# Kernel tuning notes

Measured on AMD Instinct MI355X. Metric: run time of the kernel, lower is better.

## Reference

```python
import jax, jax.numpy as jnp
import numpy as np

SCALE = 0.1  # FullAttention(0.1) binds scale positionally

def setup_inputs() -> dict:
    key = jax.random.key(0)
    k1, k2, k3, k4, k5 = jax.random.split(key, 5)
    B, H, L, E = 128, 16, 64, 128
    C = H * E  # in_channel = 2048
    return {
        "queries": jax.random.normal(k1, (B, H, L, E), dtype=jnp.float32),
        "keys": jax.random.normal(k2, (B, H, L, E), dtype=jnp.float32),
        "values": jax.random.normal(k3, (B, H, L, E), dtype=jnp.float32),
        "W": jax.random.normal(k4, (C, C), dtype=jnp.float32) * (1.0 / np.sqrt(C)),
        "b": jax.random.normal(k5, (C,), dtype=jnp.float32) * 0.01,
    }

def reference(queries, keys, values, W, b):
    # inputs are [B, H, L, E]; module permutes to [B, L, H, E]
    q = jnp.transpose(queries, (0, 2, 1, 3))  # blhe
    k = jnp.transpose(keys, (0, 2, 1, 3))     # bshe
    v = jnp.transpose(values, (0, 2, 1, 3))   # bshd
    scores = jnp.einsum('blhe,bshe->bhls', q, k)
    A = jax.nn.softmax(SCALE * scores, axis=-1)  # dropout is identity in eval
    V = jnp.einsum('bhls,bshd->blhd', A, v)
    B_, L, H, D = V.shape
    out = V.reshape(-1, 64, H * D)  # view(-1, 64, in_channel)
    return out @ W.T + b
```

## Files before the change

### kernel.cpp

```cpp
#include <hip/hip_runtime.h>
#include <hip/hip_bf16.h>
#include <stdint.h>

typedef __bf16 bf16_t;
typedef __bf16 bf16x4 __attribute__((ext_vector_type(4)));
typedef __bf16 bf16x8 __attribute__((ext_vector_type(8)));
typedef float  f32x4  __attribute__((ext_vector_type(4)));

#define AS1 __attribute__((address_space(1)))
#define AS3 __attribute__((address_space(3)))

__device__ __forceinline__ void gld_lds16(const void* gp, void* lp) {
    __builtin_amdgcn_global_load_lds((const AS1 unsigned int*)gp,
                                     (AS3 unsigned int*)lp, 16, 0, 0);
}

__device__ __forceinline__ bf16_t bhi(float v) { return (bf16_t)v; }
__device__ __forceinline__ bf16_t blo(float v) {
    return (bf16_t)(v - (float)((bf16_t)v));
}

__global__ __launch_bounds__(256) void wconv_kernel(const float* __restrict__ W,
                                                    bf16_t* __restrict__ Wb) {
    const int i = (blockIdx.x * 256 + threadIdx.x) * 4;
    const float4 f = *(const float4*)&W[i];
    bf16x4 v = { (bf16_t)f.x, (bf16_t)f.y, (bf16_t)f.z, (bf16_t)f.w };
    *(bf16x4*)&Wb[i] = v;
}

#define QK_LD 136
#define VT_LD 72
#define SF_LD 65

__global__ __launch_bounds__(256) void attn_kernel(const float* __restrict__ Q,
                                                   const float* __restrict__ K,
                                                   const float* __restrict__ V,
                                                   bf16_t* __restrict__ X) {
    __shared__ __align__(16) char smem[53248];
    bf16_t* Qs = (bf16_t*)smem;
    bf16_t* Ks = (bf16_t*)(smem + 17408);
    bf16_t* Vt = (bf16_t*)(smem + 34816);
    float*  Sf = (float*)smem;
    bf16_t* Ps = (bf16_t*)(smem + 17408);

    const int bh   = blockIdx.x;
    const int b    = bh >> 4;
    const int h    = bh & 15;
    const int t    = threadIdx.x;
    const int w    = t >> 6;
    const int lane = t & 63;
    const int row16 = lane & 15;
    const int quad  = lane >> 4;

    const float* Qg = Q + (size_t)bh * 8192;
    const float* Kg = K + (size_t)bh * 8192;
    const float* Vg = V + (size_t)bh * 8192;

    const int r  = t >> 2;
    const int c0 = (t & 3) * 32;

    float qv[32], kv[32];
#pragma unroll
    for (int j = 0; j < 8; ++j) {
        const int c = c0 + 4 * j;
        *(float4*)&qv[4 * j] = *(const float4*)&Qg[r * 128 + c];
        *(float4*)&kv[4 * j] = *(const float4*)&Kg[r * 128 + c];
        const float4 v4 = *(const float4*)&Vg[r * 128 + c];
        Vt[(c + 0) * VT_LD + r] = (bf16_t)v4.x;
        Vt[(c + 1) * VT_LD + r] = (bf16_t)v4.y;
        Vt[(c + 2) * VT_LD + r] = (bf16_t)v4.z;
        Vt[(c + 3) * VT_LD + r] = (bf16_t)v4.w;
    }

#define STAGE(slot, vals, CONV)                                            \
    {                                                                      \
        _Pragma("unroll")                                                  \
        for (int j = 0; j < 8; ++j) {                                      \
            const int c = c0 + 4 * j;                                      \
            bf16x4 o = { CONV(vals[4*j+0]), CONV(vals[4*j+1]),             \
                         CONV(vals[4*j+2]), CONV(vals[4*j+3]) };           \
            *(bf16x4*)&slot[r * QK_LD + c] = o;                            \
        }                                                                  \
    }

    f32x4 accS[4];
#pragma unroll
    for (int ni = 0; ni < 4; ++ni) accS[ni] = (f32x4){0.f, 0.f, 0.f, 0.f};

#define SCORE_PASS()                                                       \
    {                                                                      \
        _Pragma("unroll")                                                  \
        for (int kb = 0; kb < 4; ++kb) {                                   \
            const bf16x8 a = *(const bf16x8*)&Qs[(16*w + row16)*QK_LD + 32*kb + 8*quad]; \
            _Pragma("unroll")                                              \
            for (int ni = 0; ni < 4; ++ni) {                               \
                const bf16x8 bb = *(const bf16x8*)&Ks[(16*ni + row16)*QK_LD + 32*kb + 8*quad]; \
                accS[ni] = __builtin_amdgcn_mfma_f32_16x16x32_bf16(a, bb, accS[ni], 0, 0, 0); \
            }                                                              \
        }                                                                  \
    }

    STAGE(Qs, qv, bhi)
    STAGE(Ks, kv, bhi)
    __syncthreads();
    SCORE_PASS()
    __syncthreads();
    STAGE(Ks, kv, blo)
    __syncthreads();
    SCORE_PASS()
    __syncthreads();
    STAGE(Qs, qv, blo)
    __syncthreads();
    SCORE_PASS()
    __syncthreads();
    STAGE(Ks, kv, bhi)
    __syncthreads();
    SCORE_PASS()
    __syncthreads();

#pragma unroll
    for (int ni = 0; ni < 4; ++ni)
#pragma unroll
        for (int rr = 0; rr < 4; ++rr)
            Sf[(16 * w + 4 * quad + rr) * SF_LD + 16 * ni + row16] = accS[ni][rr];
    __syncthreads();

    {
        const int c16 = (t & 3) * 16;
        float x[16];
        float mx = -1e30f;
#pragma unroll
        for (int j = 0; j < 16; ++j) {
            x[j] = Sf[r * SF_LD + c16 + j] * 0.1f;
            mx = fmaxf(mx, x[j]);
        }
        mx = fmaxf(mx, __shfl_xor(mx, 1));
        mx = fmaxf(mx, __shfl_xor(mx, 2));
        float sum = 0.f;
#pragma unroll
        for (int j = 0; j < 16; ++j) {
            x[j] = exp2f((x[j] - mx) * 1.44269504088896f);
            sum += x[j];
        }
        sum += __shfl_xor(sum, 1);
        sum += __shfl_xor(sum, 2);
        const float inv = 1.0f / sum;
#pragma unroll
        for (int j4 = 0; j4 < 4; ++j4) {
            bf16x4 p = { (bf16_t)(x[4 * j4 + 0] * inv), (bf16_t)(x[4 * j4 + 1] * inv),
                         (bf16_t)(x[4 * j4 + 2] * inv), (bf16_t)(x[4 * j4 + 3] * inv) };
            *(bf16x4*)&Ps[r * VT_LD + c16 + 4 * j4] = p;
        }
    }
    __syncthreads();

    f32x4 accO[8];
#pragma unroll
    for (int ni = 0; ni < 8; ++ni) accO[ni] = (f32x4){0.f, 0.f, 0.f, 0.f};
#pragma unroll
    for (int kb = 0; kb < 2; ++kb) {
        const bf16x8 a = *(const bf16x8*)&Ps[(16 * w + row16) * VT_LD + 32 * kb + 8 * quad];
#pragma unroll
        for (int ni = 0; ni < 8; ++ni) {
            const bf16x8 bb = *(const bf16x8*)&Vt[(16 * ni + row16) * VT_LD + 32 * kb + 8 * quad];
            accO[ni] = __builtin_amdgcn_mfma_f32_16x16x32_bf16(a, bb, accO[ni], 0, 0, 0);
        }
    }

    bf16_t* Xrow = X + (size_t)b * 64 * 2048 + h * 128;
#pragma unroll
    for (int ni = 0; ni < 8; ++ni)
#pragma unroll
        for (int rr = 0; rr < 4; ++rr) {
            const int l = 16 * w + 4 * quad + rr;
            const int d = 16 * ni + row16;
            Xrow[(size_t)l * 2048 + d] = (bf16_t)accO[ni][rr];
        }
}

__global__ __launch_bounds__(256) void gemm_kernel(const bf16_t* __restrict__ X,
                                                   const bf16_t* __restrict__ Wb,
                                                   const float* __restrict__ bias,
                                                   float* __restrict__ out) {
    __shared__ bf16_t As[128 * 32];
    __shared__ bf16_t Bs[128 * 32];

    const int t    = threadIdx.x;
    const int w    = t >> 6;
    const int lane = t & 63;
    const int row16 = lane & 15;
    const int quad  = lane >> 4;
    const int m0 = blockIdx.y * 128;
    const int n0 = blockIdx.x * 128;
    const int wm = w >> 1;
    const int wn = w & 1;

    const int srow = 32 * w + (lane >> 2);
    const int scol = (lane & 3) * 8;
    const bf16_t* gA = X  + (size_t)(m0 + srow) * 2048 + scol;
    const bf16_t* gB = Wb + (size_t)(n0 + srow) * 2048 + scol;
    bf16_t* lA0 = &As[(32 * w) * 32];
    bf16_t* lA1 = &As[(32 * w + 16) * 32];
    bf16_t* lB0 = &Bs[(32 * w) * 32];
    bf16_t* lB1 = &Bs[(32 * w + 16) * 32];

    f32x4 acc[4][4];
#pragma unroll
    for (int mi = 0; mi < 4; ++mi)
#pragma unroll
        for (int ni = 0; ni < 4; ++ni) acc[mi][ni] = (f32x4){0.f, 0.f, 0.f, 0.f};

    for (int kb = 0; kb < 64; ++kb) {
        const int k0 = kb * 32;
        __syncthreads();
        gld_lds16(gA + k0, lA0);
        gld_lds16(gA + 16 * 2048 + k0, lA1);
        gld_lds16(gB + k0, lB0);
        gld_lds16(gB + 16 * 2048 + k0, lB1);
        __syncthreads();

        bf16x8 a[4], bb[4];
#pragma unroll
        for (int mi = 0; mi < 4; ++mi)
            a[mi] = *(const bf16x8*)&As[(64 * wm + 16 * mi + row16) * 32 + 8 * quad];
#pragma unroll
        for (int ni = 0; ni < 4; ++ni)
            bb[ni] = *(const bf16x8*)&Bs[(64 * wn + 16 * ni + row16) * 32 + 8 * quad];
#pragma unroll
        for (int mi = 0; mi < 4; ++mi)
#pragma unroll
            for (int ni = 0; ni < 4; ++ni)
                acc[mi][ni] = __builtin_amdgcn_mfma_f32_16x16x32_bf16(a[mi], bb[ni], acc[mi][ni], 0, 0, 0);
    }

    const int nb = n0 + 64 * wn;
    float br[4];
#pragma unroll
    for (int ni = 0; ni < 4; ++ni) br[ni] = bias[nb + 16 * ni + row16];
#pragma unroll
    for (int mi = 0; mi < 4; ++mi)
#pragma unroll
        for (int ni = 0; ni < 4; ++ni)
#pragma unroll
            for (int rr = 0; rr < 4; ++rr) {
                const int m = m0 + 64 * wm + 16 * mi + 4 * quad + rr;
                const int n = nb + 16 * ni + row16;
                out[(size_t)m * 2048 + n] = acc[mi][ni][rr] + br[ni];
            }
}

extern "C" void kernel_launch(void* const* d_in, const int* in_sizes, int n_in,
                              void* d_out, int out_size, void* d_ws, size_t ws_size,
                              hipStream_t stream) {
    const float* Q    = (const float*)d_in[0];
    const float* K    = (const float*)d_in[1];
    const float* V    = (const float*)d_in[2];
    const float* W    = (const float*)d_in[3];
    const float* bias = (const float*)d_in[4];

    bf16_t* Xws = (bf16_t*)d_ws;
    bf16_t* Wb  = (bf16_t*)((char*)d_ws + (size_t)8192 * 2048 * 2);
    float*  out = (float*)d_out;

    wconv_kernel<<<4096, 256, 0, stream>>>(W, Wb);
    attn_kernel<<<2048, 256, 0, stream>>>(Q, K, V, Xws);
    gemm_kernel<<<dim3(16, 64), 256, 0, stream>>>(Xws, Wb, bias, out);
}
```

Baseline: 325.0 us.

## Trim split-bf16 score passes, coalesce attention output, widen GEMM K-tile with swizzle

The attention kernel drops the lo×lo score pass, going from four MFMA passes to three (hi·hi, hi·lo, lo·hi). It also stages the output tile through LDS so global writes become 16-byte vector stores instead of scattered 2-byte stores. The GEMM doubles its K-tile to 64 with an XOR-swizzled LDS layout to avoid bank conflicts, halving the number of barrier pairs. It also swaps the grid order so consecutive blocks share a W column tile, and adds an occupancy hint. Dropping the lo×lo term slightly changes the score precision, which stays negligible at bf16-split accuracy.

```diff
diff --git a/kernel.cpp b/kernel.cpp
--- a/kernel.cpp
+++ b/kernel.cpp
@@ -42,6 +42,7 @@
     bf16_t* Vt = (bf16_t*)(smem + 34816);
     float*  Sf = (float*)smem;
     bf16_t* Ps = (bf16_t*)(smem + 17408);
+    bf16_t* Ob = (bf16_t*)smem;
 
     const int bh   = blockIdx.x;
     const int b    = bh >> 4;
@@ -101,19 +102,15 @@
     }
 
     STAGE(Qs, qv, bhi)
+    STAGE(Ks, kv, blo)
+    __syncthreads();
+    SCORE_PASS()
+    __syncthreads();
     STAGE(Ks, kv, bhi)
     __syncthreads();
     SCORE_PASS()
     __syncthreads();
-    STAGE(Ks, kv, blo)
-    __syncthreads();
-    SCORE_PASS()
-    __syncthreads();
     STAGE(Qs, qv, blo)
-    __syncthreads();
-    SCORE_PASS()
-    __syncthreads();
-    STAGE(Ks, kv, bhi)
     __syncthreads();
     SCORE_PASS()
     __syncthreads();
@@ -167,42 +164,57 @@
         }
     }
 
-    bf16_t* Xrow = X + (size_t)b * 64 * 2048 + h * 128;
 #pragma unroll
     for (int ni = 0; ni < 8; ++ni)
 #pragma unroll
-        for (int rr = 0; rr < 4; ++rr) {
-            const int l = 16 * w + 4 * quad + rr;
-            const int d = 16 * ni + row16;
-            Xrow[(size_t)l * 2048 + d] = (bf16_t)accO[ni][rr];
-        }
-}
-
-__global__ __launch_bounds__(256) void gemm_kernel(const bf16_t* __restrict__ X,
-                                                   const bf16_t* __restrict__ Wb,
-                                                   const float* __restrict__ bias,
-                                                   float* __restrict__ out) {
-    __shared__ bf16_t As[128 * 32];
-    __shared__ bf16_t Bs[128 * 32];
+        for (int rr = 0; rr < 4; ++rr)
+            Ob[(16 * w + 4 * quad + rr) * QK_LD + 16 * ni + row16] = (bf16_t)accO[ni][rr];
+    __syncthreads();
+
+    {
+        bf16_t* Xrow = X + (size_t)b * 64 * 2048 + h * 128 + (size_t)r * 2048;
+#pragma unroll
+        for (int j = 0; j < 4; ++j) {
+            *(bf16x8*)&Xrow[c0 + 8 * j] = *(const bf16x8*)&Ob[r * QK_LD + c0 + 8 * j];
+        }
+    }
+}
+
+__global__ __launch_bounds__(256, 4) void gemm_kernel(const bf16_t* __restrict__ X,
+                                                      const bf16_t* __restrict__ Wb,
+                                                      const float* __restrict__ bias,
+                                                      float* __restrict__ out) {
+    __shared__ bf16_t As[128 * 64];
+    __shared__ bf16_t Bs[128 * 64];
 
     const int t    = threadIdx.x;
     const int w    = t >> 6;
     const int lane = t & 63;
     const int row16 = lane & 15;
     const int quad  = lane >> 4;
-    const int m0 = blockIdx.y * 128;
-    const int n0 = blockIdx.x * 128;
+    const int m0 = blockIdx.x * 128;
+    const int n0 = blockIdx.y * 128;
     const int wm = w >> 1;
     const int wn = w & 1;
 
-    const int srow = 32 * w + (lane >> 2);
-    const int scol = (lane & 3) * 8;
-    const bf16_t* gA = X  + (size_t)(m0 + srow) * 2048 + scol;
-    const bf16_t* gB = Wb + (size_t)(n0 + srow) * 2048 + scol;
-    bf16_t* lA0 = &As[(32 * w) * 32];
-    bf16_t* lA1 = &As[(32 * w + 16) * 32];
-    bf16_t* lB0 = &Bs[(32 * w) * 32];
-    bf16_t* lB1 = &Bs[(32 * w + 16) * 32];
+    const int row8 = lane >> 3;
+    const int scol = 8 * ((lane & 7) ^ (row8 & 7));
+    const bf16_t* gA = X  + (size_t)(m0 + 32 * w + row8) * 2048 + scol;
+    const bf16_t* gB = Wb + (size_t)(n0 + 32 * w + row8) * 2048 + scol;
+    bf16_t* lA = &As[(32 * w) * 64];
+    bf16_t* lB = &Bs[(32 * w) * 64];
+
+    const int sw = row16 & 7;
+    int aoff[4][2], boff[4][2];
+#pragma unroll
+    for (int mi = 0; mi < 4; ++mi)
+#pragma unroll
+        for (int kk = 0; kk < 2; ++kk) {
+            const int ar = 64 * wm + 16 * mi + row16;
+            const int br = 64 * wn + 16 * mi + row16;
+            aoff[mi][kk] = ar * 64 + 8 * ((4 * kk + quad) ^ sw);
+            boff[mi][kk] = br * 64 + 8 * ((4 * kk + quad) ^ sw);
+        }
 
     f32x4 acc[4][4];
 #pragma unroll
@@ -210,27 +222,29 @@
 #pragma unroll
         for (int ni = 0; ni < 4; ++ni) acc[mi][ni] = (f32x4){0.f, 0.f, 0.f, 0.f};
 
-    for (int kb = 0; kb < 64; ++kb) {
-        const int k0 = kb * 32;
+    for (int kb = 0; kb < 32; ++kb) {
+        const int k0 = kb * 64;
         __syncthreads();
-        gld_lds16(gA + k0, lA0);
-        gld_lds16(gA + 16 * 2048 + k0, lA1);
-        gld_lds16(gB + k0, lB0);
-        gld_lds16(gB + 16 * 2048 + k0, lB1);
+#pragma unroll
+        for (int i = 0; i < 4; ++i) {
+            gld_lds16(gA + (size_t)(8 * i) * 2048 + k0, lA + (8 * i) * 64);
+            gld_lds16(gB + (size_t)(8 * i) * 2048 + k0, lB + (8 * i) * 64);
+        }
         __syncthreads();
 
-        bf16x8 a[4], bb[4];
-#pragma unroll
-        for (int mi = 0; mi < 4; ++mi)
-            a[mi] = *(const bf16x8*)&As[(64 * wm + 16 * mi + row16) * 32 + 8 * quad];
-#pragma unroll
-        for (int ni = 0; ni < 4; ++ni)
-            bb[ni] = *(const bf16x8*)&Bs[(64 * wn + 16 * ni + row16) * 32 + 8 * quad];
-#pragma unroll
-        for (int mi = 0; mi < 4; ++mi)
-#pragma unroll
-            for (int ni = 0; ni < 4; ++ni)
-                acc[mi][ni] = __builtin_amdgcn_mfma_f32_16x16x32_bf16(a[mi], bb[ni], acc[mi][ni], 0, 0, 0);
+#pragma unroll
+        for (int kk = 0; kk < 2; ++kk) {
+            bf16x8 a[4], bb[4];
+#pragma unroll
+            for (int mi = 0; mi < 4; ++mi) a[mi]  = *(const bf16x8*)&As[aoff[mi][kk]];
+#pragma unroll
+            for (int ni = 0; ni < 4; ++ni) bb[ni] = *(const bf16x8*)&Bs[boff[ni][kk]];
+#pragma unroll
+            for (int mi = 0; mi < 4; ++mi)
+#pragma unroll
+                for (int ni = 0; ni < 4; ++ni)
+                    acc[mi][ni] = __builtin_amdgcn_mfma_f32_16x16x32_bf16(a[mi], bb[ni], acc[mi][ni], 0, 0, 0);
+        }
     }
 
     const int nb = n0 + 64 * wn;
@@ -264,5 +278,5 @@
 
     wconv_kernel<<<4096, 256, 0, stream>>>(W, Wb);
     attn_kernel<<<2048, 256, 0, stream>>>(Q, K, V, Xws);
-    gemm_kernel<<<dim3(16, 64), 256, 0, stream>>>(Xws, Wb, bias, out);
-}
+    gemm_kernel<<<dim3(64, 16), 256, 0, stream>>>(Xws, Wb, bias, out);
+}
```

Result: faster. 298.6 us (-8.1%).
